# Kernel tuning notes

Hardware: AMD Instinct MI355X
Metric: run time of the kernel (lower is better)

## Reference

```python
import jax, jax.numpy as jnp
import numpy as np

N, F_IN, HID, NH1, NCLS = 8192, 256, 64, 4, 16
LRELU_ALPHA = 0.2  # tf.nn.leaky_relu default


def setup_inputs() -> dict:
    key = jax.random.key(0)
    ks = jax.random.split(key, 12)
    s = 0.05
    seq = jax.random.normal(ks[0], (1, N, F_IN), jnp.float32)
    # sparse-ish adjacency -> additive mask bias (0 on edges, -1e9 elsewhere)
    adj = jax.random.uniform(ks[1], (N, N)) < 0.005
    adj = adj | jnp.eye(N, dtype=bool)
    bias_mat = jnp.where(adj, 0.0, -1e9).astype(jnp.float32)[None]  # [1,N,N]
    return {
        "seq": seq,
        "bias_mat": bias_mat,
        "W1": jax.random.normal(ks[2], (NH1, F_IN, HID), jnp.float32) * s,
        "a1_src": jax.random.normal(ks[3], (NH1, HID, 1), jnp.float32) * s,
        "a1_dst": jax.random.normal(ks[4], (NH1, HID, 1), jnp.float32) * s,
        "b1_src": jnp.zeros((NH1, 1), jnp.float32),
        "b1_dst": jnp.zeros((NH1, 1), jnp.float32),
        "bias1": jnp.zeros((NH1, HID), jnp.float32),
        "W2": jax.random.normal(ks[5], (1, NH1 * HID, NCLS), jnp.float32) * s,
        "a2_src": jax.random.normal(ks[6], (1, NCLS, 1), jnp.float32) * s,
        "a2_dst": jax.random.normal(ks[7], (1, NCLS, 1), jnp.float32) * s,
        "b2_src": jnp.zeros((1, 1), jnp.float32),
        "b2_dst": jnp.zeros((1, 1), jnp.float32),
        "bias2": jnp.zeros((1, NCLS), jnp.float32),
    }


def _gat_layer(x, bias_mat, W, a_src, a_dst, b_src, b_dst, bias_out):
    # x: [N, Fin]; W: [nh, Fin, H]; bias_mat: [1, N, N]
    fts = jnp.einsum('nf,hfd->hnd', x, W)                      # Conv1D(k=1, no bias)
    f1 = jnp.einsum('hnd,hdo->hno', fts, a_src) + b_src[:, None, :]  # [nh,N,1]
    f2 = jnp.einsum('hnd,hdo->hno', fts, a_dst) + b_dst[:, None, :]  # [nh,N,1]
    logits = f1 + jnp.swapaxes(f2, 1, 2)                       # [nh,N,N]
    coefs = jax.nn.softmax(jax.nn.leaky_relu(logits, LRELU_ALPHA) + bias_mat, axis=-1)
    vals = jnp.einsum('hnm,hmd->hnd', coefs, fts)              # [nh,N,H]
    return vals + bias_out[:, None, :]


def reference(seq, bias_mat, W1, a1_src, a1_dst, b1_src, b1_dst, bias1,
              W2, a2_src, a2_dst, b2_src, b2_dst, bias2):
    x = seq[0]  # [N, F_IN]; batch dim is 1
    # layer 1: NH1 heads, elu activation, concat over heads
    h = jax.nn.elu(_gat_layer(x, bias_mat, W1, a1_src, a1_dst, b1_src, b1_dst, bias1))
    h1 = jnp.transpose(h, (1, 0, 2)).reshape(N, NH1 * HID)     # tf.concat(heads, -1)
    # output layer: 1 head, identity activation, averaged over final heads (=1)
    out = _gat_layer(h1, bias_mat, W2, a2_src, a2_dst, b2_src, b2_dst, bias2)
    logits = out[0] / 1.0                                      # add_n/final_sum
    return logits[None]  # [1, N, NCLS]
```

## Files before the change

### kernel.cpp

```cpp
#include <hip/hip_runtime.h>
#include <hip/hip_bf16.h>
#include <math.h>

#define NN    8192
#define FIN   256
#define HID   64
#define NH    4
#define NC    16
#define MAXD  128
#define ALPHA 0.2f
#define KC    32

typedef float nfloat4 __attribute__((ext_vector_type(4)));
__device__ __forceinline__ float4 ldnt4(const float4* p) {
    nfloat4 v = __builtin_nontemporal_load((const nfloat4*)p);
    return make_float4(v.x, v.y, v.z, v.w);
}
__device__ __forceinline__ ushort f2bf(float x) {
    __hip_bfloat16 h = __float2bfloat16(x);
    return *reinterpret_cast<ushort*>(&h);
}
__device__ __forceinline__ float bfhi(unsigned u) { return __uint_as_float(u & 0xffff0000u); }
__device__ __forceinline__ float bflo(unsigned u) { return __uint_as_float(u << 16); }

__device__ __forceinline__ void scan_row(
    int row, int lane, int* colsW,
    const float* __restrict__ bias, int* __restrict__ deg, int* __restrict__ cols)
{
    const unsigned long long lt = (1ull << lane) - 1ull;
    colsW[lane] = 0; colsW[64 + lane] = 0;
    const float4* rp = (const float4*)(bias + (size_t)row * NN);
    float4 vv[8];
    #pragma unroll
    for (int k = 0; k < 8; ++k) vv[k] = ldnt4(rp + k*64 + lane);
    int base = 0;
    #pragma unroll
    for (int s = 0; s < 4; ++s) {
        #pragma unroll
        for (int k = 0; k < 8; ++k) {
            const float4 v = vv[k];
            if (s < 3) vv[k] = ldnt4(rp + ((s+1)*8 + k)*64 + lane);
            const unsigned long long m0 = __ballot(v.x == 0.f);
            const unsigned long long m1 = __ballot(v.y == 0.f);
            const unsigned long long m2 = __ballot(v.z == 0.f);
            const unsigned long long m3 = __ballot(v.w == 0.f);
            const int cb = ((s*8 + k)*64 + lane)*4;
            int p = base + __popcll(m0&lt) + __popcll(m1&lt)
                         + __popcll(m2&lt) + __popcll(m3&lt);
            if (v.x == 0.f) { if (p < MAXD) colsW[p] = cb;     ++p; }
            if (v.y == 0.f) { if (p < MAXD) colsW[p] = cb + 1; ++p; }
            if (v.z == 0.f) { if (p < MAXD) colsW[p] = cb + 2; ++p; }
            if (v.w == 0.f) { if (p < MAXD) colsW[p] = cb + 3; ++p; }
            base += __popcll(m0) + __popcll(m1) + __popcll(m2) + __popcll(m3);
        }
    }
    const int d = base < MAXD ? base : MAXD;
    if (lane == 0) deg[row] = d;
    cols[(size_t)row*MAXD + lane]      = colsW[lane];
    cols[(size_t)row*MAXD + 64 + lane] = colsW[64 + lane];
}

__global__ __launch_bounds__(256) void k_gemm_scan(
    const float* __restrict__ seq, const float* __restrict__ W1,
    const float* __restrict__ a1s, const float* __restrict__ a1d,
    const float* __restrict__ b1s, const float* __restrict__ b1d,
    const float* __restrict__ bias,
    ushort* __restrict__ fts1g, float* __restrict__ f1v, float* __restrict__ f2v,
    int* __restrict__ deg, int* __restrict__ cols)
{
    __shared__ union {
        struct { float xsT[KC][68]; float w[KC][68]; } g;
        struct { float r1[64][17];  float r2[64][17]; } gr;
        int colsS[4][MAXD];
    } S;
    const int t = threadIdx.x, bid = blockIdx.x;
    const int w = t >> 6, lane = t & 63;

    if (bid >= 512) {
        scan_row((bid - 512)*4 + w, lane, &S.colsS[w][0], bias, deg, cols);
        return;
    }
    const int head = bid & 3, rowbase = (bid >> 2) * 64;
    const int tr = t >> 4, tc = t & 15;

    float acc[4][4] = {};
    for (int kc = 0; kc < FIN / KC; ++kc) {
        #pragma unroll
        for (int i = 0; i < 2; ++i) {
            const int lin = t + i*256;
            const int row = lin >> 3, kq = lin & 7;
            const float4 v = *(const float4*)(seq + (size_t)(rowbase + row)*FIN + kc*KC + kq*4);
            S.g.xsT[kq*4+0][row] = v.x;
            S.g.xsT[kq*4+1][row] = v.y;
            S.g.xsT[kq*4+2][row] = v.z;
            S.g.xsT[kq*4+3][row] = v.w;
        }
        #pragma unroll
        for (int i = 0; i < 2; ++i) {
            const int lin = t + i*256;
            const int k = lin >> 4, dq = lin & 15;
            *(float4*)&S.g.w[k][dq*4] =
                *(const float4*)(W1 + ((size_t)head*FIN + kc*KC + k)*HID + dq*4);
        }
        __syncthreads();
        #pragma unroll 8
        for (int k = 0; k < KC; ++k) {
            const float4 aa = *(const float4*)&S.g.xsT[k][tr*4];
            const float4 bb = *(const float4*)&S.g.w[k][tc*4];
            acc[0][0] += aa.x*bb.x; acc[0][1] += aa.x*bb.y; acc[0][2] += aa.x*bb.z; acc[0][3] += aa.x*bb.w;
            acc[1][0] += aa.y*bb.x; acc[1][1] += aa.y*bb.y; acc[1][2] += aa.y*bb.z; acc[1][3] += aa.y*bb.w;
            acc[2][0] += aa.z*bb.x; acc[2][1] += aa.z*bb.y; acc[2][2] += aa.z*bb.z; acc[2][3] += aa.z*bb.w;
            acc[3][0] += aa.w*bb.x; acc[3][1] += aa.w*bb.y; acc[3][2] += aa.w*bb.z; acc[3][3] += aa.w*bb.w;
        }
        __syncthreads();
    }
    float p1[4], p2[4];
    #pragma unroll
    for (int i = 0; i < 4; ++i) {
        const int node = rowbase + tr*4 + i;
        ushort4 o;
        o.x = f2bf(acc[i][0]); o.y = f2bf(acc[i][1]);
        o.z = f2bf(acc[i][2]); o.w = f2bf(acc[i][3]);
        *(ushort4*)&fts1g[(size_t)node*(NH*HID) + head*HID + tc*4] = o;
        float s1 = 0.f, s2 = 0.f;
        #pragma unroll
        for (int j = 0; j < 4; ++j) {
            s1 += acc[i][j] * a1s[head*HID + tc*4 + j];
            s2 += acc[i][j] * a1d[head*HID + tc*4 + j];
        }
        p1[i] = s1; p2[i] = s2;
    }
    #pragma unroll
    for (int i = 0; i < 4; ++i) {
        S.gr.r1[tr*4 + i][tc] = p1[i];
        S.gr.r2[tr*4 + i][tc] = p2[i];
    }
    __syncthreads();
    if (t < 64) {
        float s1 = b1s[head], s2 = b1d[head];
        #pragma unroll
        for (int q = 0; q < 16; ++q) { s1 += S.gr.r1[t][q]; s2 += S.gr.r2[t][q]; }
        f1v[(rowbase + t)*NH + head] = s1;
        f2v[(rowbase + t)*NH + head] = s2;
    }
}

__global__ __launch_bounds__(256) void k_attn1(
    const ushort* __restrict__ fts1g, const float* __restrict__ f1v4,
    const float* __restrict__ f2v4, const float* __restrict__ bias1,
    const float* __restrict__ W2, const float* __restrict__ a2s,
    const float* __restrict__ a2d, const float* __restrict__ b2s,
    const float* __restrict__ b2d,
    const int* __restrict__ deg, const int* __restrict__ cols,
    float* __restrict__ fts2, float* __restrict__ g1, float* __restrict__ g2)
{
    __shared__ int    colsS[4][MAXD];
    __shared__ float4 coefS[4][MAXD];
    __shared__ float  h1S[4][NH*68];

    const int t = threadIdx.x, w = t >> 6, lane = t & 63;
    const int row = blockIdx.x*4 + w;
    int* colsW = &colsS[w][0];
    float4* coefW = &coefS[w][0];
    float* h1W = &h1S[w][0];

    const int d = deg[row];
    const int c0 = cols[(size_t)row*MAXD + lane];
    const int c1 = cols[(size_t)row*MAXD + 64 + lane];
    colsW[lane] = c0; colsW[64 + lane] = c1;

    const float4 f1 = *(const float4*)(f1v4 + (size_t)row*NH);
    float4 s0 = make_float4(-1e30f,-1e30f,-1e30f,-1e30f), s1 = s0;
    if (lane < d) {
        const float4 F = *(const float4*)(f2v4 + (size_t)c0*NH);
        float x;
        x = f1.x + F.x; s0.x = x > 0.f ? x : ALPHA*x;
        x = f1.y + F.y; s0.y = x > 0.f ? x : ALPHA*x;
        x = f1.z + F.z; s0.z = x > 0.f ? x : ALPHA*x;
        x = f1.w + F.w; s0.w = x > 0.f ? x : ALPHA*x;
    }
    if (lane + 64 < d) {
        const float4 F = *(const float4*)(f2v4 + (size_t)c1*NH);
        float x;
        x = f1.x + F.x; s1.x = x > 0.f ? x : ALPHA*x;
        x = f1.y + F.y; s1.y = x > 0.f ? x : ALPHA*x;
        x = f1.z + F.z; s1.z = x > 0.f ? x : ALPHA*x;
        x = f1.w + F.w; s1.w = x > 0.f ? x : ALPHA*x;
    }
    float4 m;
    m.x = fmaxf(s0.x, s1.x); m.y = fmaxf(s0.y, s1.y);
    m.z = fmaxf(s0.z, s1.z); m.w = fmaxf(s0.w, s1.w);
    #pragma unroll
    for (int off = 32; off; off >>= 1) {
        m.x = fmaxf(m.x, __shfl_xor(m.x, off));
        m.y = fmaxf(m.y, __shfl_xor(m.y, off));
        m.z = fmaxf(m.z, __shfl_xor(m.z, off));
        m.w = fmaxf(m.w, __shfl_xor(m.w, off));
    }
    float4 p0 = make_float4(0,0,0,0), p1 = p0;
    if (lane < d) {
        p0.x = expf(s0.x - m.x); p0.y = expf(s0.y - m.y);
        p0.z = expf(s0.z - m.z); p0.w = expf(s0.w - m.w);
    }
    if (lane + 64 < d) {
        p1.x = expf(s1.x - m.x); p1.y = expf(s1.y - m.y);
        p1.z = expf(s1.z - m.z); p1.w = expf(s1.w - m.w);
    }
    coefW[lane] = p0; coefW[64 + lane] = p1;
    float4 sum;
    sum.x = p0.x + p1.x; sum.y = p0.y + p1.y;
    sum.z = p0.z + p1.z; sum.w = p0.w + p1.w;
    #pragma unroll
    for (int off = 32; off; off >>= 1) {
        sum.x += __shfl_xor(sum.x, off);
        sum.y += __shfl_xor(sum.y, off);
        sum.z += __shfl_xor(sum.z, off);
        sum.w += __shfl_xor(sum.w, off);
    }
    const int h = lane >> 4;
    const float invh = (h==0) ? 1.f/sum.x : (h==1) ? 1.f/sum.y
                     : (h==2) ? 1.f/sum.z : 1.f/sum.w;

    float a0 = 0.f, a1 = 0.f, a2 = 0.f, a3 = 0.f;
    #pragma unroll 8
    for (int e = 0; e < d; ++e) {
        const float4 q4 = coefW[e];
        const float cf = (h==0) ? q4.x : (h==1) ? q4.y : (h==2) ? q4.z : q4.w;
        const uint2 q = *(const uint2*)(fts1g + (size_t)colsW[e]*(NH*HID) + lane*4);
        a0 += cf * bflo(q.x); a1 += cf * bfhi(q.x);
        a2 += cf * bflo(q.y); a3 += cf * bfhi(q.y);
    }
    const float4 bv = *(const float4*)(bias1 + lane*4);
    float4 ev;
    float v;
    v = a0*invh + bv.x; ev.x = v > 0.f ? v : expm1f(v);
    v = a1*invh + bv.y; ev.y = v > 0.f ? v : expm1f(v);
    v = a2*invh + bv.z; ev.z = v > 0.f ? v : expm1f(v);
    v = a3*invh + bv.w; ev.w = v > 0.f ? v : expm1f(v);
    *(float4*)&h1W[h*68 + (lane & 15)*4] = ev;

    const int part = lane >> 4, c = lane & 15;
    float s = 0.f;
    #pragma unroll 8
    for (int q = 0; q < 64; ++q)
        s += h1W[part*68 + q] * W2[(part*64 + q)*NC + c];
    s += __shfl_xor(s, 16);
    s += __shfl_xor(s, 32);
    if (lane < NC) fts2[(size_t)row*NC + lane] = s;

    float t1 = (lane < NC) ? s * a2s[lane] : 0.f;
    float t2 = (lane < NC) ? s * a2d[lane] : 0.f;
    #pragma unroll
    for (int off = 8; off; off >>= 1) {
        t1 += __shfl_xor(t1, off);
        t2 += __shfl_xor(t2, off);
    }
    if (lane == 0) { g1[row] = t1 + b2s[0]; g2[row] = t2 + b2d[0]; }
}

__global__ __launch_bounds__(256) void k_attn2(
    const float* __restrict__ fts2, const float* __restrict__ g1,
    const float* __restrict__ g2, const float* __restrict__ bias2,
    const int* __restrict__ deg, const int* __restrict__ cols,
    float* __restrict__ out)
{
    __shared__ int   colsS[4][MAXD];
    __shared__ float coefS[4][MAXD];
    const int t = threadIdx.x, w = t >> 6, lane = t & 63;
    const int i = blockIdx.x*4 + w;
    const int d = deg[i];
    for (int e = lane; e < MAXD; e += 64) colsS[w][e] = (e < d) ? cols[(size_t)i*MAXD + e] : 0;

    const float g1i = g1[i];
    float sc0 = -1e30f, sc1 = -1e30f;
    if (lane < d)      { const float x = g1i + g2[colsS[w][lane]];    sc0 = x > 0.f ? x : ALPHA*x; }
    if (lane + 64 < d) { const float x = g1i + g2[colsS[w][lane+64]]; sc1 = x > 0.f ? x : ALPHA*x; }
    float m = fmaxf(sc0, sc1);
    #pragma unroll
    for (int off = 32; off; off >>= 1) m = fmaxf(m, __shfl_xor(m, off));
    const float p0 = (lane      < d) ? expf(sc0 - m) : 0.f;
    const float p1 = (lane + 64 < d) ? expf(sc1 - m) : 0.f;
    coefS[w][lane] = p0; coefS[w][lane + 64] = p1;
    float sum = p0 + p1;
    #pragma unroll
    for (int off = 32; off; off >>= 1) sum += __shfl_xor(sum, off);
    const float inv = 1.f / sum;

    const int eg = lane >> 4, c = lane & 15;
    float acc = 0.f;
    #pragma unroll 2
    for (int e0 = 0; e0 < d; e0 += 4) {
        const int e = e0 + eg;
        if (e < d) acc += coefS[w][e] * fts2[(size_t)colsS[w][e]*NC + c];
    }
    acc += __shfl_xor(acc, 16);
    acc += __shfl_xor(acc, 32);
    if (lane < NC) out[(size_t)i*NC + lane] = acc*inv + bias2[lane];
}

extern "C" void kernel_launch(void* const* d_in, const int* in_sizes, int n_in,
                              void* d_out, int out_size, void* d_ws, size_t ws_size,
                              hipStream_t stream)
{
    const float* seq   = (const float*)d_in[0];
    const float* bias  = (const float*)d_in[1];
    const float* W1    = (const float*)d_in[2];
    const float* a1s   = (const float*)d_in[3];
    const float* a1d   = (const float*)d_in[4];
    const float* b1s   = (const float*)d_in[5];
    const float* b1d   = (const float*)d_in[6];
    const float* bias1 = (const float*)d_in[7];
    const float* W2    = (const float*)d_in[8];
    const float* a2s   = (const float*)d_in[9];
    const float* a2d   = (const float*)d_in[10];
    const float* b2s   = (const float*)d_in[11];
    const float* b2d   = (const float*)d_in[12];
    const float* bias2 = (const float*)d_in[13];

    char* ws = (char*)d_ws;
    int*    deg   = (int*)ws;    ws += (size_t)NN * 4;
    int*    cols  = (int*)ws;    ws += (size_t)NN * MAXD * 4;
    ushort* fts1g = (ushort*)ws; ws += (size_t)NN * NH * HID * 2;
    float*  f1v   = (float*)ws;  ws += (size_t)NN * NH * 4;
    float*  f2v   = (float*)ws;  ws += (size_t)NN * NH * 4;
    float*  fts2  = (float*)ws;  ws += (size_t)NN * NC * 4;
    float*  g1    = (float*)ws;  ws += (size_t)NN * 4;
    float*  g2    = (float*)ws;  ws += (size_t)NN * 4;

    hipLaunchKernelGGL(k_gemm_scan, dim3(512 + NN/4), dim3(256), 0, stream,
                       seq, W1, a1s, a1d, b1s, b1d, bias,
                       fts1g, f1v, f2v, deg, cols);
    hipLaunchKernelGGL(k_attn1, dim3(NN/4), dim3(256), 0, stream,
                       fts1g, f1v, f2v, bias1, W2, a2s, a2d, b2s, b2d,
                       deg, cols, fts2, g1, g2);
    hipLaunchKernelGGL(k_attn2, dim3(NN/4), dim3(256), 0, stream,
                       fts2, g1, g2, bias2, deg, cols, (float*)d_out);
}
```

Baseline: 92.10 us.

## Fuse adjacency scan into layer-1 attention with online softmax

Moves the bias-matrix scan out of the GEMM kernel and into the layer-1 attention kernel. Each wave now streams two rows of the mask and processes each edge as it is found, using an online-softmax update instead of a separate max/sum pass over stored coefficients. The GEMM kernel no longer carries the scan blocks, so the 256 MB mask read is no longer overlapped with the GEMM. The edge loop is serialized per set bit with exp rescaling on every edge, which adds dependent latency and scalar work per edge.

```diff
diff --git a/kernel.cpp b/kernel.cpp
--- a/kernel.cpp
+++ b/kernel.cpp
@@ -10,6 +10,7 @@
 #define MAXD  128
 #define ALPHA 0.2f
 #define KC    32
+#define RPW   2
 
 typedef float nfloat4 __attribute__((ext_vector_type(4)));
 __device__ __forceinline__ float4 ldnt4(const float4* p) {
@@ -23,63 +24,17 @@
 __device__ __forceinline__ float bfhi(unsigned u) { return __uint_as_float(u & 0xffff0000u); }
 __device__ __forceinline__ float bflo(unsigned u) { return __uint_as_float(u << 16); }
 
-__device__ __forceinline__ void scan_row(
-    int row, int lane, int* colsW,
-    const float* __restrict__ bias, int* __restrict__ deg, int* __restrict__ cols)
-{
-    const unsigned long long lt = (1ull << lane) - 1ull;
-    colsW[lane] = 0; colsW[64 + lane] = 0;
-    const float4* rp = (const float4*)(bias + (size_t)row * NN);
-    float4 vv[8];
-    #pragma unroll
-    for (int k = 0; k < 8; ++k) vv[k] = ldnt4(rp + k*64 + lane);
-    int base = 0;
-    #pragma unroll
-    for (int s = 0; s < 4; ++s) {
-        #pragma unroll
-        for (int k = 0; k < 8; ++k) {
-            const float4 v = vv[k];
-            if (s < 3) vv[k] = ldnt4(rp + ((s+1)*8 + k)*64 + lane);
-            const unsigned long long m0 = __ballot(v.x == 0.f);
-            const unsigned long long m1 = __ballot(v.y == 0.f);
-            const unsigned long long m2 = __ballot(v.z == 0.f);
-            const unsigned long long m3 = __ballot(v.w == 0.f);
-            const int cb = ((s*8 + k)*64 + lane)*4;
-            int p = base + __popcll(m0&lt) + __popcll(m1&lt)
-                         + __popcll(m2&lt) + __popcll(m3&lt);
-            if (v.x == 0.f) { if (p < MAXD) colsW[p] = cb;     ++p; }
-            if (v.y == 0.f) { if (p < MAXD) colsW[p] = cb + 1; ++p; }
-            if (v.z == 0.f) { if (p < MAXD) colsW[p] = cb + 2; ++p; }
-            if (v.w == 0.f) { if (p < MAXD) colsW[p] = cb + 3; ++p; }
-            base += __popcll(m0) + __popcll(m1) + __popcll(m2) + __popcll(m3);
-        }
-    }
-    const int d = base < MAXD ? base : MAXD;
-    if (lane == 0) deg[row] = d;
-    cols[(size_t)row*MAXD + lane]      = colsW[lane];
-    cols[(size_t)row*MAXD + 64 + lane] = colsW[64 + lane];
-}
-
-__global__ __launch_bounds__(256) void k_gemm_scan(
+__global__ __launch_bounds__(256) void k_gemm(
     const float* __restrict__ seq, const float* __restrict__ W1,
     const float* __restrict__ a1s, const float* __restrict__ a1d,
     const float* __restrict__ b1s, const float* __restrict__ b1d,
-    const float* __restrict__ bias,
-    ushort* __restrict__ fts1g, float* __restrict__ f1v, float* __restrict__ f2v,
-    int* __restrict__ deg, int* __restrict__ cols)
+    ushort* __restrict__ fts1g, float* __restrict__ f1v, float* __restrict__ f2v)
 {
     __shared__ union {
         struct { float xsT[KC][68]; float w[KC][68]; } g;
         struct { float r1[64][17];  float r2[64][17]; } gr;
-        int colsS[4][MAXD];
     } S;
     const int t = threadIdx.x, bid = blockIdx.x;
-    const int w = t >> 6, lane = t & 63;
-
-    if (bid >= 512) {
-        scan_row((bid - 512)*4 + w, lane, &S.colsS[w][0], bias, deg, cols);
-        return;
-    }
     const int head = bid & 3, rowbase = (bid >> 2) * 64;
     const int tr = t >> 4, tc = t & 15;
 
@@ -145,117 +100,114 @@
     }
 }
 
-__global__ __launch_bounds__(256) void k_attn1(
-    const ushort* __restrict__ fts1g, const float* __restrict__ f1v4,
-    const float* __restrict__ f2v4, const float* __restrict__ bias1,
-    const float* __restrict__ W2, const float* __restrict__ a2s,
-    const float* __restrict__ a2d, const float* __restrict__ b2s,
-    const float* __restrict__ b2d,
-    const int* __restrict__ deg, const int* __restrict__ cols,
+__global__ __launch_bounds__(256) void k_scan_attn(
+    const float* __restrict__ bias, const ushort* __restrict__ fts1g,
+    const float* __restrict__ f1v4, const float* __restrict__ f2v4,
+    const float* __restrict__ bias1, const float* __restrict__ W2,
+    const float* __restrict__ a2s, const float* __restrict__ a2d,
+    const float* __restrict__ b2s, const float* __restrict__ b2d,
+    int* __restrict__ deg, int* __restrict__ cols,
     float* __restrict__ fts2, float* __restrict__ g1, float* __restrict__ g2)
 {
-    __shared__ int    colsS[4][MAXD];
-    __shared__ float4 coefS[4][MAXD];
-    __shared__ float  h1S[4][NH*68];
+    __shared__ int   colsS[4][MAXD];
+    __shared__ float h1S[4][NH*68];
 
     const int t = threadIdx.x, w = t >> 6, lane = t & 63;
-    const int row = blockIdx.x*4 + w;
-    int* colsW = &colsS[w][0];
-    float4* coefW = &coefS[w][0];
-    float* h1W = &h1S[w][0];
-
-    const int d = deg[row];
-    const int c0 = cols[(size_t)row*MAXD + lane];
-    const int c1 = cols[(size_t)row*MAXD + 64 + lane];
-    colsW[lane] = c0; colsW[64 + lane] = c1;
-
-    const float4 f1 = *(const float4*)(f1v4 + (size_t)row*NH);
-    float4 s0 = make_float4(-1e30f,-1e30f,-1e30f,-1e30f), s1 = s0;
-    if (lane < d) {
-        const float4 F = *(const float4*)(f2v4 + (size_t)c0*NH);
-        float x;
-        x = f1.x + F.x; s0.x = x > 0.f ? x : ALPHA*x;
-        x = f1.y + F.y; s0.y = x > 0.f ? x : ALPHA*x;
-        x = f1.z + F.z; s0.z = x > 0.f ? x : ALPHA*x;
-        x = f1.w + F.w; s0.w = x > 0.f ? x : ALPHA*x;
-    }
-    if (lane + 64 < d) {
-        const float4 F = *(const float4*)(f2v4 + (size_t)c1*NH);
-        float x;
-        x = f1.x + F.x; s1.x = x > 0.f ? x : ALPHA*x;
-        x = f1.y + F.y; s1.y = x > 0.f ? x : ALPHA*x;
-        x = f1.z + F.z; s1.z = x > 0.f ? x : ALPHA*x;
-        x = f1.w + F.w; s1.w = x > 0.f ? x : ALPHA*x;
-    }
-    float4 m;
-    m.x = fmaxf(s0.x, s1.x); m.y = fmaxf(s0.y, s1.y);
-    m.z = fmaxf(s0.z, s1.z); m.w = fmaxf(s0.w, s1.w);
-    #pragma unroll
-    for (int off = 32; off; off >>= 1) {
-        m.x = fmaxf(m.x, __shfl_xor(m.x, off));
-        m.y = fmaxf(m.y, __shfl_xor(m.y, off));
-        m.z = fmaxf(m.z, __shfl_xor(m.z, off));
-        m.w = fmaxf(m.w, __shfl_xor(m.w, off));
-    }
-    float4 p0 = make_float4(0,0,0,0), p1 = p0;
-    if (lane < d) {
-        p0.x = expf(s0.x - m.x); p0.y = expf(s0.y - m.y);
-        p0.z = expf(s0.z - m.z); p0.w = expf(s0.w - m.w);
-    }
-    if (lane + 64 < d) {
-        p1.x = expf(s1.x - m.x); p1.y = expf(s1.y - m.y);
-        p1.z = expf(s1.z - m.z); p1.w = expf(s1.w - m.w);
-    }
-    coefW[lane] = p0; coefW[64 + lane] = p1;
-    float4 sum;
-    sum.x = p0.x + p1.x; sum.y = p0.y + p1.y;
-    sum.z = p0.z + p1.z; sum.w = p0.w + p1.w;
-    #pragma unroll
-    for (int off = 32; off; off >>= 1) {
-        sum.x += __shfl_xor(sum.x, off);
-        sum.y += __shfl_xor(sum.y, off);
-        sum.z += __shfl_xor(sum.z, off);
-        sum.w += __shfl_xor(sum.w, off);
-    }
     const int h = lane >> 4;
-    const float invh = (h==0) ? 1.f/sum.x : (h==1) ? 1.f/sum.y
-                     : (h==2) ? 1.f/sum.z : 1.f/sum.w;
-
+    int*   colsW = &colsS[w][0];
+    float* h1W   = &h1S[w][0];
+
+    const int rowbase = (blockIdx.x*4 + w) * RPW;
+
+    int   cnt = 0;
+    float m = -1e30f, l = 0.f;
     float a0 = 0.f, a1 = 0.f, a2 = 0.f, a3 = 0.f;
-    #pragma unroll 8
-    for (int e = 0; e < d; ++e) {
-        const float4 q4 = coefW[e];
-        const float cf = (h==0) ? q4.x : (h==1) ? q4.y : (h==2) ? q4.z : q4.w;
-        const uint2 q = *(const uint2*)(fts1g + (size_t)colsW[e]*(NH*HID) + lane*4);
-        a0 += cf * bflo(q.x); a1 += cf * bfhi(q.x);
-        a2 += cf * bflo(q.y); a3 += cf * bfhi(q.y);
-    }
-    const float4 bv = *(const float4*)(bias1 + lane*4);
-    float4 ev;
-    float v;
-    v = a0*invh + bv.x; ev.x = v > 0.f ? v : expm1f(v);
-    v = a1*invh + bv.y; ev.y = v > 0.f ? v : expm1f(v);
-    v = a2*invh + bv.z; ev.z = v > 0.f ? v : expm1f(v);
-    v = a3*invh + bv.w; ev.w = v > 0.f ? v : expm1f(v);
-    *(float4*)&h1W[h*68 + (lane & 15)*4] = ev;
-
-    const int part = lane >> 4, c = lane & 15;
-    float s = 0.f;
-    #pragma unroll 8
-    for (int q = 0; q < 64; ++q)
-        s += h1W[part*68 + q] * W2[(part*64 + q)*NC + c];
-    s += __shfl_xor(s, 16);
-    s += __shfl_xor(s, 32);
-    if (lane < NC) fts2[(size_t)row*NC + lane] = s;
-
-    float t1 = (lane < NC) ? s * a2s[lane] : 0.f;
-    float t2 = (lane < NC) ? s * a2d[lane] : 0.f;
-    #pragma unroll
-    for (int off = 8; off; off >>= 1) {
-        t1 += __shfl_xor(t1, off);
-        t2 += __shfl_xor(t2, off);
-    }
-    if (lane == 0) { g1[row] = t1 + b2s[0]; g2[row] = t2 + b2d[0]; }
+    float f1h = f1v4[rowbase*NH + h];
+    colsW[lane] = 0; colsW[64 + lane] = 0;
+
+    float4 vv[8];
+    #pragma unroll
+    for (int k = 0; k < 8; ++k)
+        vv[k] = ldnt4((const float4*)(bias + (size_t)rowbase*NN) + k*64 + lane);
+
+    for (int g = 0; g < 32*RPW; ++g) {
+        const int c = g & 31;
+        const int j = g >> 5;
+        const int row = rowbase + j;
+        const float4 v = vv[g & 7];
+        const int pf = g + 8;
+        if (pf < 32*RPW) {
+            const int prow = rowbase + (pf >> 5);
+            vv[g & 7] = ldnt4((const float4*)(bias + (size_t)prow*NN) + (pf & 31)*64 + lane);
+        }
+        unsigned long long mm0 = __ballot(v.x == 0.f);
+        unsigned long long mm1 = __ballot(v.y == 0.f);
+        unsigned long long mm2 = __ballot(v.z == 0.f);
+        unsigned long long mm3 = __ballot(v.w == 0.f);
+        const int cb = c * 256;
+        #pragma unroll
+        for (int i = 0; i < 4; ++i) {
+            unsigned long long mm = (i==0)?mm0:(i==1)?mm1:(i==2)?mm2:mm3;
+            while (mm) {
+                const int b = __ffsll(mm) - 1;
+                mm &= mm - 1;
+                const int col = cb + b*4 + i;
+                if (lane == 0 && cnt < MAXD) colsW[cnt] = col;
+                ++cnt;
+                const float Fh = f2v4[col*NH + h];
+                float s = f1h + Fh; s = s > 0.f ? s : ALPHA*s;
+                const float mn = fmaxf(m, s);
+                const float fo = __expf(m - mn);
+                const float fn = __expf(s - mn);
+                m = mn;
+                l = l*fo + fn;
+                const uint2 q = *(const uint2*)(fts1g + (size_t)col*(NH*HID) + lane*4);
+                a0 = a0*fo + fn*bflo(q.x);
+                a1 = a1*fo + fn*bfhi(q.x);
+                a2 = a2*fo + fn*bflo(q.y);
+                a3 = a3*fo + fn*bfhi(q.y);
+            }
+        }
+        if (c == 31) {
+            const int d = cnt < MAXD ? cnt : MAXD;
+            cols[(size_t)row*MAXD + lane]      = colsW[lane];
+            cols[(size_t)row*MAXD + 64 + lane] = colsW[64 + lane];
+            if (lane == 0) deg[row] = d;
+            const float invl = 1.f / l;
+            const float4 bv = *(const float4*)(bias1 + lane*4);
+            float4 ev; float x;
+            x = a0*invl + bv.x; ev.x = x > 0.f ? x : expm1f(x);
+            x = a1*invl + bv.y; ev.y = x > 0.f ? x : expm1f(x);
+            x = a2*invl + bv.z; ev.z = x > 0.f ? x : expm1f(x);
+            x = a3*invl + bv.w; ev.w = x > 0.f ? x : expm1f(x);
+            *(float4*)&h1W[h*68 + (lane & 15)*4] = ev;
+
+            const int part = lane >> 4, cc = lane & 15;
+            float s2 = 0.f;
+            #pragma unroll 8
+            for (int q2 = 0; q2 < 64; ++q2)
+                s2 += h1W[part*68 + q2] * W2[(part*64 + q2)*NC + cc];
+            s2 += __shfl_xor(s2, 16);
+            s2 += __shfl_xor(s2, 32);
+            if (lane < NC) fts2[(size_t)row*NC + lane] = s2;
+
+            float t1 = (lane < NC) ? s2 * a2s[lane] : 0.f;
+            float t2 = (lane < NC) ? s2 * a2d[lane] : 0.f;
+            #pragma unroll
+            for (int off = 8; off; off >>= 1) {
+                t1 += __shfl_xor(t1, off);
+                t2 += __shfl_xor(t2, off);
+            }
+            if (lane == 0) { g1[row] = t1 + b2s[0]; g2[row] = t2 + b2d[0]; }
+
+            if (j + 1 < RPW) {
+                cnt = 0; m = -1e30f; l = 0.f;
+                a0 = a1 = a2 = a3 = 0.f;
+                f1h = f1v4[(row + 1)*NH + h];
+                colsW[lane] = 0; colsW[64 + lane] = 0;
+            }
+        }
+    }
 }
 
 __global__ __launch_bounds__(256) void k_attn2(
@@ -327,11 +279,10 @@
     float*  g1    = (float*)ws;  ws += (size_t)NN * 4;
     float*  g2    = (float*)ws;  ws += (size_t)NN * 4;
 
-    hipLaunchKernelGGL(k_gemm_scan, dim3(512 + NN/4), dim3(256), 0, stream,
-                       seq, W1, a1s, a1d, b1s, b1d, bias,
-                       fts1g, f1v, f2v, deg, cols);
-    hipLaunchKernelGGL(k_attn1, dim3(NN/4), dim3(256), 0, stream,
-                       fts1g, f1v, f2v, bias1, W2, a2s, a2d, b2s, b2d,
+    hipLaunchKernelGGL(k_gemm, dim3(512), dim3(256), 0, stream,
+                       seq, W1, a1s, a1d, b1s, b1d, fts1g, f1v, f2v);
+    hipLaunchKernelGGL(k_scan_attn, dim3(NN/(4*RPW)), dim3(256), 0, stream,
+                       bias, fts1g, f1v, f2v, bias1, W2, a2s, a2d, b2s, b2d,
                        deg, cols, fts2, g1, g2);
     hipLaunchKernelGGL(k_attn2, dim3(NN/4), dim3(256), 0, stream,
                        fts2, g1, g2, bias2, deg, cols, (float*)d_out);
```

New measurement: 217.9 us. +136.6%, slower.

## Interleave GEMM and scan blocks and batch neighbor gathers in attn1

Applied to the files above, without the earlier changes.

The fused GEMM+scan launch now interleaves one GEMM block after every four scan blocks instead of placing all GEMM blocks first. Compute-heavy and bandwidth-heavy work should then share the CUs concurrently. In k_attn1 the neighbor aggregation loop now issues eight gathers of bf16 features before consuming them, which exposes memory-level parallelism. The cols and coefficient buffers are padded with zeros so the 8-wide batches can overrun the degree safely. The padding adds a little LDS, and the overrun entries do wasted loads of row 0.

```diff
diff --git a/kernel.cpp b/kernel.cpp
--- a/kernel.cpp
+++ b/kernel.cpp
@@ -8,6 +8,7 @@
 #define NH    4
 #define NC    16
 #define MAXD  128
+#define MAXDP 136
 #define ALPHA 0.2f
 #define KC    32
 
@@ -75,12 +76,13 @@
     } S;
     const int t = threadIdx.x, bid = blockIdx.x;
     const int w = t >> 6, lane = t & 63;
-
-    if (bid >= 512) {
-        scan_row((bid - 512)*4 + w, lane, &S.colsS[w][0], bias, deg, cols);
+    const int g5 = bid / 5, r5 = bid - g5*5;
+
+    if (r5 != 4) {
+        scan_row((g5*4 + r5)*4 + w, lane, &S.colsS[w][0], bias, deg, cols);
         return;
     }
-    const int head = bid & 3, rowbase = (bid >> 2) * 64;
+    const int head = g5 & 3, rowbase = (g5 >> 2) * 64;
     const int tr = t >> 4, tc = t & 15;
 
     float acc[4][4] = {};
@@ -154,20 +156,21 @@
     const int* __restrict__ deg, const int* __restrict__ cols,
     float* __restrict__ fts2, float* __restrict__ g1, float* __restrict__ g2)
 {
-    __shared__ int    colsS[4][MAXD];
-    __shared__ float4 coefS[4][MAXD];
+    __shared__ int    colsS[4][MAXDP];
+    __shared__ float4 coefS[4][MAXDP];
     __shared__ float  h1S[4][NH*68];
 
     const int t = threadIdx.x, w = t >> 6, lane = t & 63;
     const int row = blockIdx.x*4 + w;
-    int* colsW = &colsS[w][0];
+    int*    colsW = &colsS[w][0];
     float4* coefW = &coefS[w][0];
-    float* h1W = &h1S[w][0];
+    float*  h1W   = &h1S[w][0];
 
     const int d = deg[row];
     const int c0 = cols[(size_t)row*MAXD + lane];
     const int c1 = cols[(size_t)row*MAXD + 64 + lane];
     colsW[lane] = c0; colsW[64 + lane] = c1;
+    if (lane < MAXDP - MAXD) colsW[MAXD + lane] = 0;
 
     const float4 f1 = *(const float4*)(f1v4 + (size_t)row*NH);
     float4 s0 = make_float4(-1e30f,-1e30f,-1e30f,-1e30f), s1 = s0;
@@ -207,6 +210,7 @@
         p1.z = expf(s1.z - m.z); p1.w = expf(s1.w - m.w);
     }
     coefW[lane] = p0; coefW[64 + lane] = p1;
+    if (lane < MAXDP - MAXD) coefW[MAXD + lane] = make_float4(0,0,0,0);
     float4 sum;
     sum.x = p0.x + p1.x; sum.y = p0.y + p1.y;
     sum.z = p0.z + p1.z; sum.w = p0.w + p1.w;
@@ -220,15 +224,20 @@
     const int h = lane >> 4;
     const float invh = (h==0) ? 1.f/sum.x : (h==1) ? 1.f/sum.y
                      : (h==2) ? 1.f/sum.z : 1.f/sum.w;
+    const float* coefF = (const float*)coefW;
 
     float a0 = 0.f, a1 = 0.f, a2 = 0.f, a3 = 0.f;
-    #pragma unroll 8
-    for (int e = 0; e < d; ++e) {
-        const float4 q4 = coefW[e];
-        const float cf = (h==0) ? q4.x : (h==1) ? q4.y : (h==2) ? q4.z : q4.w;
-        const uint2 q = *(const uint2*)(fts1g + (size_t)colsW[e]*(NH*HID) + lane*4);
-        a0 += cf * bflo(q.x); a1 += cf * bfhi(q.x);
-        a2 += cf * bflo(q.y); a3 += cf * bfhi(q.y);
+    for (int e0 = 0; e0 < d; e0 += 8) {
+        uint2 qb[8];
+        #pragma unroll
+        for (int i = 0; i < 8; ++i)
+            qb[i] = *(const uint2*)(fts1g + (size_t)colsW[e0+i]*(NH*HID) + lane*4);
+        #pragma unroll
+        for (int i = 0; i < 8; ++i) {
+            const float cf = coefF[(e0+i)*4 + h];
+            a0 += cf * bflo(qb[i].x); a1 += cf * bfhi(qb[i].x);
+            a2 += cf * bflo(qb[i].y); a3 += cf * bfhi(qb[i].y);
+        }
     }
     const float4 bv = *(const float4*)(bias1 + lane*4);
     float4 ev;
@@ -327,7 +336,7 @@
     float*  g1    = (float*)ws;  ws += (size_t)NN * 4;
     float*  g2    = (float*)ws;  ws += (size_t)NN * 4;
 
-    hipLaunchKernelGGL(k_gemm_scan, dim3(512 + NN/4), dim3(256), 0, stream,
+    hipLaunchKernelGGL(k_gemm_scan, dim3(2560), dim3(256), 0, stream,
                        seq, W1, a1s, a1d, b1s, b1d, bias,
                        fts1g, f1v, f2v, deg, cols);
     hipLaunchKernelGGL(k_attn1, dim3(NN/4), dim3(256), 0, stream,
```

New measurement: 113.7 us. 23.5% more time.
